# Performance work log

Measured on AMD Instinct MI355X. Metric: run time of the kernel, lower is better.

Reference implementation:

```python
import jax, jax.numpy as jnp
import numpy as np

N_STEPS = 8   # fixed-step RK4 surrogate for diffrax Dopri5 (same RHS math)
DT = 0.01     # dt0 used by the original module


def setup_inputs() -> dict:
    key = jax.random.key(0)
    ks = jax.random.split(key, 6)
    B, N, H = 16, 512, 128
    return {
        "y0": jax.random.normal(ks[0], (B, N), jnp.float32),
        "bias": jax.random.normal(ks[1], (B, N, 1), jnp.float32),
        "data_adj": jax.random.uniform(ks[2], (B, N, N), jnp.float32),
        "k0": jax.random.normal(ks[3], (H, N, N), jnp.float32) * 0.02,
        "k1": jax.random.normal(ks[4], (H, N, H), jnp.float32) * 0.02,
        "k2": jax.random.normal(ks[5], (N, N, H), jnp.float32) * 0.02,
    }


def reference(y0, bias, data_adj, k0, k1, k2):
    b = bias[..., 0]  # squeeze(bias, -1) -> [B, N]

    def rhs(y):
        z = y[..., None]  # [B, N, 1]
        # kernel chain: einsum('ijk,lmj->ilm') per layer (k summed out)
        z = jnp.einsum('ijk,lmj->ilm', z, k0)  # [B, H, N]
        z = jnp.einsum('ijk,lmj->ilm', z, k1)  # [B, H, N]
        z = jnp.einsum('ijk,lmj->ilm', z, k2)  # [B, N, N]
        z = jnp.sin(z)                          # Sine activation (dropout p=0 -> identity)
        agg = jnp.sum(data_adj * z, axis=-1)    # adjacency-masked reduction -> [B, N]
        return b - agg

    def step(y, _):
        r1 = rhs(y)
        r2 = rhs(y + 0.5 * DT * r1)
        r3 = rhs(y + 0.5 * DT * r2)
        r4 = rhs(y + DT * r3)
        y_new = y + (DT / 6.0) * (r1 + 2.0 * r2 + 2.0 * r3 + r4)
        return y_new, y_new

    _, ys = jax.lax.scan(step, y0, None, length=N_STEPS)
    return ys  # [N_STEPS, B, N] trajectory (SaveAt(ts=ts) analogue)
```

## Files before the change

kernel.cpp:

```cpp
#include <hip/hip_runtime.h>
#include <hip/hip_bf16.h>

typedef int int4v __attribute__((ext_vector_type(4)));
typedef long long i64;
typedef long long i64x2 __attribute__((ext_vector_type(2)));
typedef unsigned long long u64;
typedef unsigned int u32;

#define DT 0.01f

__device__ __forceinline__ float fast_sin(float x) {
  const float INVPI = 0.3183098861837907f;
  float n = rintf(x * INVPI);
  int ni = (int)n;
  float r = fmaf(n, -3.140625f, x);
  r = fmaf(n, -9.6765358979e-4f, r);
  float s = r * r;
  float p = fmaf(s, -2.5052108e-8f, 2.7557319e-6f);
  p = fmaf(s, p, -1.9841270e-4f);
  p = fmaf(s, p, 8.3333333e-3f);
  p = fmaf(s, p, -1.6666667e-1f);
  float res = fmaf(r * s, p, r);
  return (ni & 1) ? -res : res;
}

typedef float f32x16 __attribute__((ext_vector_type(16)));
__device__ __forceinline__ void sload4(const float* p, f32x16& a, f32x16& b,
                                       f32x16& c, f32x16& d) {
  asm volatile(
      "s_load_dwordx16 %0, %4, 0\n\t"
      "s_load_dwordx16 %1, %4, 0x40\n\t"
      "s_load_dwordx16 %2, %4, 0x80\n\t"
      "s_load_dwordx16 %3, %4, 0xc0\n\t"
      "s_waitcnt lgkmcnt(0)"
      : "=s"(a), "=s"(b), "=s"(c), "=s"(d)
      : "s"(p));
}

__global__ __launch_bounds__(256) void kPrep1(const float* __restrict__ k0,
                                              float* __restrict__ K0p) {
  const int id = (blockIdx.x & 255) * 256 + threadIdx.x;
  const int p = blockIdx.x >> 8;
  const int h = id >> 9, j = id & 511;
  const float* q = k0 + (size_t)h * 262144 + (size_t)(p * 256) * 512 + j;
  float s = 0.f;
  for (int m = 0; m < 256; ++m) s += q[(size_t)m * 512];
  K0p[p * 65536 + id] = s;
}

__global__ __launch_bounds__(256) void kPrep2(const float* __restrict__ k1,
                                              float* __restrict__ K1s) {
  int t = blockIdx.x * 256 + threadIdx.x;
  int h = t >> 7, j = t & 127;
  const float* p = k1 + (size_t)h * 65536 + j;
  float s = 0.f;
  for (int m = 0; m < 512; ++m) s += p[(size_t)m * 128];
  K1s[t] = s;
}

__global__ __launch_bounds__(256) void kPrep3(const float* __restrict__ K0p,
                                              const float* __restrict__ K1s,
                                              float* __restrict__ M) {
  int t = blockIdx.x * 256 + threadIdx.x;
  int l = t >> 9, j = t & 511;
  float s = 0.f;
#pragma unroll 8
  for (int h = 0; h < 128; ++h)
    s = fmaf(K1s[l * 128 + h], K0p[h * 512 + j] + K0p[65536 + h * 512 + j], s);
  M[t] = s;
}

__global__ __launch_bounds__(256) void kConvRow(const float* __restrict__ k2,
                                                i64x2* __restrict__ kF2,
                                                float* __restrict__ rowinv,
                                                float* __restrict__ crow) {
  const int t = threadIdx.x;
  const int row = blockIdx.x * 16 + (t >> 4);
  const int seg = t & 15;
  const float* src = k2 + (size_t)row * 128 + seg * 8;
  const float4 a = *(const float4*)(src);
  const float4 b = *(const float4*)(src + 4);
  float m = fmaxf(fmaxf(fmaxf(fabsf(a.x), fabsf(a.y)), fmaxf(fabsf(a.z), fabsf(a.w))),
                  fmaxf(fmaxf(fabsf(b.x), fabsf(b.y)), fmaxf(fabsf(b.z), fabsf(b.w))));
#pragma unroll
  for (int off = 8; off > 0; off >>= 1) m = fmaxf(m, __shfl_xor(m, off, 64));
  const float scale = m > 0.f ? 32767.0f / m : 0.f;
  if (seg == 0) rowinv[row] = m > 0.f ? m / 32767.0f : 0.f;
  const float v[8] = {a.x, a.y, a.z, a.w, b.x, b.y, b.z, b.w};
  u64 ph = 0, pl = 0;
  int csum = 0;
#pragma unroll
  for (int i = 0; i < 8; ++i) {
    const int q = (int)rintf(v[i] * scale);
    const int kh = q >> 8;
    const int kl = (q & 255) - 128;
    ph |= (u64)(unsigned char)(signed char)kh << (8 * i);
    pl |= (u64)(unsigned char)(signed char)kl << (8 * i);
    csum += q - 128;
  }
  i64x2 wv;
  wv.x = (i64)ph;
  wv.y = (i64)pl;
  kF2[((size_t)(row >> 4) * 4 + (seg >> 2)) * 64 + (seg & 3) * 16 + (row & 15)] = wv;
#pragma unroll
  for (int off = 8; off > 0; off >>= 1) csum += __shfl_xor(csum, off, 64);
  if (seg == 0) crow[row] = 32896.f * (float)csum;
}

__global__ __launch_bounds__(256) void kA2(
    const float* __restrict__ y0, const float* __restrict__ bias,
    const float* __restrict__ M, const float* __restrict__ aggp,
    float* __restrict__ ybuf, float* __restrict__ racc,
    float* __restrict__ s2T, float* __restrict__ out,
    int stage, int step) {
  __shared__ float ystage[512];
  const int b = blockIdx.x >> 4, lg = blockIdx.x & 15, t = threadIdx.x;
  const float* ycur = ybuf + (step & 1) * 8192;
  float* ynext = ybuf + ((step + 1) & 1) * 8192;

  for (int i = t; i < 512; i += 256) {
    const int idx = b * 512 + i;
    const bool own = (i >> 5) == lg;
    float ys;
    if (stage == 0) {
      ys = y0[idx];
      if (own) ynext[idx] = ys;
    } else {
      const float r = bias[idx] - (aggp[idx] + aggp[8192 + idx]);
      const float yb = ycur[idx];
      if (stage == 1) {
        ys = fmaf(0.5f * DT, r, yb);
        if (own) racc[idx] = r;
      } else if (stage == 2) {
        ys = fmaf(0.5f * DT, r, yb);
        if (own) racc[idx] = racc[idx] + 2.f * r;
      } else if (stage == 3) {
        ys = fmaf(DT, r, yb);
        if (own) racc[idx] = racc[idx] + 2.f * r;
      } else {
        ys = yb + (DT / 6.f) * (racc[idx] + r);
        if (own) { ynext[idx] = ys; out[step * 8192 + idx] = ys; }
      }
    }
    ystage[i] = ys;
  }
  __syncthreads();

  const int g = t >> 5, u = t & 31;
  const int l = lg * 8 + g;
  const float* Mrow = M + l * 512;
  const int i0 = u * 16;
  float p = 0.f;
#pragma unroll
  for (int k = 0; k < 4; ++k) {
    const int off = ((u + k) & 3) << 2;
    const float4 mv = *(const float4*)(Mrow + i0 + off);
    const float4 yv = *(const float4*)(ystage + i0 + off);
    p = fmaf(mv.x, yv.x, p);
    p = fmaf(mv.y, yv.y, p);
    p = fmaf(mv.z, yv.z, p);
    p = fmaf(mv.w, yv.w, p);
  }
#pragma unroll
  for (int off = 16; off > 0; off >>= 1) p += __shfl_down(p, off, 32);
  if (u == 0) s2T[l * 16 + b] = p;
}

__global__ __launch_bounds__(256) void kBi8(
    const i64x2* __restrict__ kF2,
    const float* __restrict__ adj, const float* __restrict__ s2T,
    const float* __restrict__ rowinv, const float* __restrict__ crow,
    float* __restrict__ aggp) {
  __shared__ __align__(8) signed char sqA[16][136];
  __shared__ __align__(8) signed char sqB[16][136];
  __shared__ __align__(8) signed char sqC[16][136];
  __shared__ float sred[16][16];
  __shared__ float scaleL[16], sinvLs[16], cbLs[16];
  __shared__ float part[64];
  const int t = threadIdx.x;
  const int b16 = t & 15, jg = t >> 4;

  float mx = 0.f;
#pragma unroll
  for (int i = 0; i < 8; ++i)
    mx = fmaxf(mx, fabsf(s2T[(jg * 8 + i) * 16 + b16]));
  sred[jg][b16] = mx;
  __syncthreads();
  if (t < 16) {
    float m = 0.f;
#pragma unroll
    for (int g = 0; g < 16; ++g) m = fmaxf(m, sred[g][t]);
    scaleL[t] = m > 0.f ? 8388607.f / m : 0.f;
    sinvLs[t] = m > 0.f ? m / 8388607.f : 0.f;
  }
  __syncthreads();
  {
    const float sc = scaleL[b16];
    u64 pa = 0, pb = 0, pc = 0;
    int ps2 = 0, psm = 0, psl = 0;
#pragma unroll
    for (int i = 0; i < 8; ++i) {
      int q = (int)rintf(s2T[(jg * 8 + i) * 16 + b16] * sc);
      q = q > 8388607 ? 8388607 : (q < -8388607 ? -8388607 : q);
      const int h = q >> 16;
      const int m = ((q >> 8) & 255) - 128;
      const int lo = (q & 255) - 128;
      pa |= (u64)(unsigned char)(signed char)h << (8 * i);
      pb |= (u64)(unsigned char)(signed char)m << (8 * i);
      pc |= (u64)(unsigned char)(signed char)lo << (8 * i);
      ps2 += h; psm += m; psl += lo;
    }
    *(u64*)&sqA[b16][jg * 8] = pa;
    *(u64*)&sqB[b16][jg * 8] = pb;
    *(u64*)&sqC[b16][jg * 8] = pc;
    sred[jg][b16] = 8388608.f * (float)ps2 + 32768.f * (float)psm + 128.f * (float)psl;
  }
  __syncthreads();
  if (t < 16) {
    float s = 0.f;
#pragma unroll
    for (int g = 0; g < 16; ++g) s += sred[g][t];
    cbLs[t] = s + 538968064.f;
  }
  __syncthreads();

  const int lane = t & 63, w = t >> 6;
  const int bb = lane & 15, kg = lane >> 4;
  i64 bA[4], bB[4], bC[4];
#pragma unroll
  for (int c = 0; c < 4; ++c) {
    const int kb = c * 32 + kg * 8;
    bA[c] = *(const i64*)&sqA[bb][kb];
    bB[c] = *(const i64*)&sqB[bb][kb];
    bC[c] = *(const i64*)&sqC[bb][kb];
  }
  const float sb = sinvLs[bb], cbb = cbLs[bb];

  const int rid0 = blockIdx.x * 256;
  const int l = rid0 >> 9;
  const int half = blockIdx.x & 1;

  float bacc = 0.f;
#pragma unroll
  for (int tt = 0; tt < 4; ++tt) {
    const int ridT = rid0 + w * 64 + tt * 16;
    const size_t tile = (size_t)(ridT >> 4);
    i64 ah[4], al[4];
#pragma unroll
    for (int c = 0; c < 4; ++c) {
      const i64x2 v = kF2[(tile * 4 + c) * 64 + lane];
      ah[c] = v.x;
      al[c] = v.y;
    }
    int4v Ga = {0, 0, 0, 0}, Gb = {0, 0, 0, 0}, Gc = {0, 0, 0, 0}, Gd = {0, 0, 0, 0};
#pragma unroll
    for (int c = 0; c < 4; ++c) {
      Ga = __builtin_amdgcn_mfma_i32_16x16x32_i8(ah[c], bA[c], Ga, 0, 0, 0);
      Gb = __builtin_amdgcn_mfma_i32_16x16x32_i8(ah[c], bB[c], Gb, 0, 0, 0);
      Gb = __builtin_amdgcn_mfma_i32_16x16x32_i8(al[c], bA[c], Gb, 0, 0, 0);
      Gc = __builtin_amdgcn_mfma_i32_16x16x32_i8(ah[c], bC[c], Gc, 0, 0, 0);
      Gc = __builtin_amdgcn_mfma_i32_16x16x32_i8(al[c], bB[c], Gc, 0, 0, 0);
      Gd = __builtin_amdgcn_mfma_i32_16x16x32_i8(al[c], bC[c], Gd, 0, 0, 0);
    }
    const int rbase = ridT + kg * 4;
    const float4 cr = *(const float4*)(crow + rbase);
    const float4 ri = *(const float4*)(rowinv + rbase);
    const float4 ad = *(const float4*)(adj + (size_t)bb * 262144 + rbase);
    const float crA[4] = {cr.x, cr.y, cr.z, cr.w};
    const float riA[4] = {ri.x, ri.y, ri.z, ri.w};
    const float adA[4] = {ad.x, ad.y, ad.z, ad.w};
    float ts = 0.f;
#pragma unroll
    for (int r = 0; r < 4; ++r) {
      const float dq = 16777216.f * (float)Ga[r] + 65536.f * (float)Gb[r] +
                       256.f * (float)Gc[r] + (float)Gd[r] + crA[r] + cbb;
      ts += adA[r] * fast_sin(dq * (riA[r] * sb));
    }
    ts += __shfl_xor(ts, 16, 64);
    ts += __shfl_xor(ts, 32, 64);
    bacc += ts;
  }
  if (lane < 16) part[w * 16 + lane] = bacc;
  __syncthreads();
  if (t < 16) {
    float ssum = part[t] + part[16 + t] + part[32 + t] + part[48 + t];
    aggp[half * 8192 + t * 512 + l] = ssum;
  }
}

__global__ __launch_bounds__(256) void kBf32(
    const float* __restrict__ k2, const float* __restrict__ adj,
    const float* __restrict__ s2T, float* __restrict__ aggp) {
  __shared__ float lk[256 * 36];
  __shared__ float part[64];
  const int t = threadIdx.x;
  const int rid0 = blockIdx.x * 256;
  const int rid = rid0 + t;
  const int l = rid0 >> 9;
  const int half = blockIdx.x & 1;

  float dot[16];
#pragma unroll
  for (int b = 0; b < 16; ++b) dot[b] = 0.f;

  for (int c = 0; c < 4; ++c) {
    __syncthreads();
#pragma unroll
    for (int k = 0; k < 8; ++k) {
      const int f = k * 256 + t, row = f >> 3, e = f & 7;
      const float4 v = *(const float4*)(k2 + (size_t)(rid0 + row) * 128 + c * 32 + e * 4);
      *(float4*)(lk + row * 36 + e * 4) = v;
    }
    __syncthreads();
    const float* myrow = lk + t * 36;
#pragma unroll
    for (int q = 0; q < 8; ++q) {
      const float4 kv = *(const float4*)(myrow + q * 4);
      f32x16 sa, sb, sc, sd;
      sload4(s2T + (c * 32 + q * 4) * 16, sa, sb, sc, sd);
#pragma unroll
      for (int b = 0; b < 16; ++b) dot[b] = fmaf(sa[b], kv.x, dot[b]);
#pragma unroll
      for (int b = 0; b < 16; ++b) dot[b] = fmaf(sb[b], kv.y, dot[b]);
#pragma unroll
      for (int b = 0; b < 16; ++b) dot[b] = fmaf(sc[b], kv.z, dot[b]);
#pragma unroll
      for (int b = 0; b < 16; ++b) dot[b] = fmaf(sd[b], kv.w, dot[b]);
    }
  }

#pragma unroll
  for (int b = 0; b < 16; ++b) {
    float v = adj[(size_t)b * 262144 + rid] * fast_sin(dot[b]);
#pragma unroll
    for (int off = 32; off > 0; off >>= 1) v += __shfl_down(v, off, 64);
    if ((t & 63) == 0) part[(t >> 6) * 16 + b] = v;
  }
  __syncthreads();
  if (t < 16) {
    float ssum = part[t] + part[16 + t] + part[32 + t] + part[48 + t];
    aggp[half * 8192 + t * 512 + l] = ssum;
  }
}

extern "C" void kernel_launch(void* const* d_in, const int* in_sizes, int n_in,
                              void* d_out, int out_size, void* d_ws, size_t ws_size,
                              hipStream_t stream) {
  const float* y0   = (const float*)d_in[0];
  const float* bias = (const float*)d_in[1];
  const float* adj  = (const float*)d_in[2];
  const float* k0   = (const float*)d_in[3];
  const float* k1   = (const float*)d_in[4];
  const float* k2   = (const float*)d_in[5];
  float* out = (float*)d_out;

  float* w      = (float*)d_ws;
  float* K0p    = w;
  float* K1s    = w + 131072;
  float* M      = w + 147456;
  float* s2T    = w + 212992;
  float* ybuf   = w + 215040;
  float* racc   = w + 231424;
  float* aggp   = w + 239616;
  float* rowinv = w + 256000;
  float* crow   = w + 518144;
  i64x2* kF2    = (i64x2*)(w + 780288);
  const bool useI8 =
      ws_size >= (size_t)780288 * 4 + (size_t)2 * 33554432;

  kPrep1<<<512, 256, 0, stream>>>(k0, K0p);
  kPrep2<<<64, 256, 0, stream>>>(k1, K1s);
  kPrep3<<<256, 256, 0, stream>>>(K0p, K1s, M);
  if (useI8) kConvRow<<<16384, 256, 0, stream>>>(k2, kF2, rowinv, crow);

  kA2<<<256, 256, 0, stream>>>(y0, bias, M, aggp, ybuf, racc, s2T, out, 0, -1);

  for (int step = 0; step < 8; ++step) {
    for (int stage = 1; stage <= 4; ++stage) {
      if (useI8)
        kBi8<<<1024, 256, 0, stream>>>(kF2, adj, s2T, rowinv, crow, aggp);
      else
        kBf32<<<1024, 256, 0, stream>>>(k2, adj, s2T, aggp);
      kA2<<<256, 256, 0, stream>>>(y0, bias, M, aggp, ybuf, racc, s2T, out, stage, step);
    }
  }
}
```

Measured before the change: 770.9 us.

## Quantize s2 in producer kernel using a precomputed norm bound, not per block

```diff
diff --git a/kernel.cpp b/kernel.cpp
--- a/kernel.cpp
+++ b/kernel.cpp
@@ -70,6 +70,26 @@
   M[t] = s;
 }
 
+__global__ __launch_bounds__(1024) void kNorm(const float* __restrict__ M,
+                                              float* __restrict__ Mnorm) {
+  __shared__ float red[128];
+  const int t = threadIdx.x;
+  const int l = t >> 3, seg = t & 7;
+  const float* row = M + l * 512 + seg * 64;
+  float s = 0.f;
+#pragma unroll 8
+  for (int i = 0; i < 64; ++i) s += fabsf(row[i]);
+#pragma unroll
+  for (int off = 4; off > 0; off >>= 1) s += __shfl_down(s, off, 8);
+  if (seg == 0) red[l] = s;
+  __syncthreads();
+  if (t == 0) {
+    float m = 0.f;
+    for (int i = 0; i < 128; ++i) m = fmaxf(m, red[i]);
+    Mnorm[0] = m;
+  }
+}
+
 __global__ __launch_bounds__(256) void kConvRow(const float* __restrict__ k2,
                                                 i64x2* __restrict__ kF2,
                                                 float* __restrict__ rowinv,
@@ -111,13 +131,21 @@
     const float* __restrict__ y0, const float* __restrict__ bias,
     const float* __restrict__ M, const float* __restrict__ aggp,
     float* __restrict__ ybuf, float* __restrict__ racc,
-    float* __restrict__ s2T, float* __restrict__ out,
+    float* __restrict__ s2T,
+    float* __restrict__ out,
+    const float* __restrict__ Mnorm,
+    signed char* __restrict__ sqG,
+    float* __restrict__ sinvB,
+    float* __restrict__ cbPart,
     int stage, int step) {
   __shared__ float ystage[512];
+  __shared__ float ymW[4];
+  __shared__ float red2[8];
   const int b = blockIdx.x >> 4, lg = blockIdx.x & 15, t = threadIdx.x;
   const float* ycur = ybuf + (step & 1) * 8192;
   float* ynext = ybuf + ((step + 1) & 1) * 8192;
 
+  float ay = 0.f;
   for (int i = t; i < 512; i += 256) {
     const int idx = b * 512 + i;
     const bool own = (i >> 5) == lg;
@@ -143,8 +171,17 @@
       }
     }
     ystage[i] = ys;
-  }
-  __syncthreads();
+    ay = fmaxf(ay, fabsf(ys));
+  }
+#pragma unroll
+  for (int off = 32; off > 0; off >>= 1) ay = fmaxf(ay, __shfl_xor(ay, off, 64));
+  if ((t & 63) == 0) ymW[t >> 6] = ay;
+  __syncthreads();
+
+  const float ymax = fmaxf(fmaxf(ymW[0], ymW[1]), fmaxf(ymW[2], ymW[3]));
+  const float bound = Mnorm[0] * ymax;
+  const float scaleB = bound > 0.f ? 8388607.f / bound : 0.f;
+  const float sinv = bound > 0.f ? bound / 8388607.f : 0.f;
 
   const int g = t >> 5, u = t & 31;
   const int l = lg * 8 + g;
@@ -163,78 +200,58 @@
   }
 #pragma unroll
   for (int off = 16; off > 0; off >>= 1) p += __shfl_down(p, off, 32);
-  if (u == 0) s2T[l * 16 + b] = p;
+  if (u == 0) {
+    s2T[l * 16 + b] = p;
+    int q = (int)rintf(p * scaleB);
+    q = q > 8388607 ? 8388607 : (q < -8388607 ? -8388607 : q);
+    const int sh = q >> 16;
+    const int sm = ((q >> 8) & 255) - 128;
+    const int sl = (q & 255) - 128;
+    sqG[b * 128 + l] = (signed char)sh;
+    sqG[2048 + b * 128 + l] = (signed char)sm;
+    sqG[4096 + b * 128 + l] = (signed char)sl;
+    red2[g] = 8388608.f * (float)sh + 32768.f * (float)sm + 128.f * (float)sl;
+  }
+  __syncthreads();
+  if (t == 0) {
+    float s = 0.f;
+#pragma unroll
+    for (int k = 0; k < 8; ++k) s += red2[k];
+    cbPart[b * 16 + lg] = s;
+    sinvB[b] = sinv;
+  }
 }
 
 __global__ __launch_bounds__(256) void kBi8(
     const i64x2* __restrict__ kF2,
-    const float* __restrict__ adj, const float* __restrict__ s2T,
+    const float* __restrict__ adj,
+    const signed char* __restrict__ sqG,
+    const float* __restrict__ sinvB, const float* __restrict__ cbPart,
     const float* __restrict__ rowinv, const float* __restrict__ crow,
     float* __restrict__ aggp) {
-  __shared__ __align__(8) signed char sqA[16][136];
-  __shared__ __align__(8) signed char sqB[16][136];
-  __shared__ __align__(8) signed char sqC[16][136];
-  __shared__ float sred[16][16];
-  __shared__ float scaleL[16], sinvLs[16], cbLs[16];
+  __shared__ float cbL[16];
   __shared__ float part[64];
   const int t = threadIdx.x;
-  const int b16 = t & 15, jg = t >> 4;
-
-  float mx = 0.f;
-#pragma unroll
-  for (int i = 0; i < 8; ++i)
-    mx = fmaxf(mx, fabsf(s2T[(jg * 8 + i) * 16 + b16]));
-  sred[jg][b16] = mx;
-  __syncthreads();
-  if (t < 16) {
-    float m = 0.f;
-#pragma unroll
-    for (int g = 0; g < 16; ++g) m = fmaxf(m, sred[g][t]);
-    scaleL[t] = m > 0.f ? 8388607.f / m : 0.f;
-    sinvLs[t] = m > 0.f ? m / 8388607.f : 0.f;
-  }
-  __syncthreads();
-  {
-    const float sc = scaleL[b16];
-    u64 pa = 0, pb = 0, pc = 0;
-    int ps2 = 0, psm = 0, psl = 0;
-#pragma unroll
-    for (int i = 0; i < 8; ++i) {
-      int q = (int)rintf(s2T[(jg * 8 + i) * 16 + b16] * sc);
-      q = q > 8388607 ? 8388607 : (q < -8388607 ? -8388607 : q);
-      const int h = q >> 16;
-      const int m = ((q >> 8) & 255) - 128;
-      const int lo = (q & 255) - 128;
-      pa |= (u64)(unsigned char)(signed char)h << (8 * i);
-      pb |= (u64)(unsigned char)(signed char)m << (8 * i);
-      pc |= (u64)(unsigned char)(signed char)lo << (8 * i);
-      ps2 += h; psm += m; psl += lo;
-    }
-    *(u64*)&sqA[b16][jg * 8] = pa;
-    *(u64*)&sqB[b16][jg * 8] = pb;
-    *(u64*)&sqC[b16][jg * 8] = pc;
-    sred[jg][b16] = 8388608.f * (float)ps2 + 32768.f * (float)psm + 128.f * (float)psl;
-  }
-  __syncthreads();
-  if (t < 16) {
-    float s = 0.f;
-#pragma unroll
-    for (int g = 0; g < 16; ++g) s += sred[g][t];
-    cbLs[t] = s + 538968064.f;
-  }
-  __syncthreads();
-
   const int lane = t & 63, w = t >> 6;
   const int bb = lane & 15, kg = lane >> 4;
+
+  if (t < 16) {
+    float s = 538968064.f;
+#pragma unroll
+    for (int g = 0; g < 16; ++g) s += cbPart[t * 16 + g];
+    cbL[t] = s;
+  }
+  __syncthreads();
+
   i64 bA[4], bB[4], bC[4];
 #pragma unroll
   for (int c = 0; c < 4; ++c) {
-    const int kb = c * 32 + kg * 8;
-    bA[c] = *(const i64*)&sqA[bb][kb];
-    bB[c] = *(const i64*)&sqB[bb][kb];
-    bC[c] = *(const i64*)&sqC[bb][kb];
-  }
-  const float sb = sinvLs[bb], cbb = cbLs[bb];
+    const int kb = bb * 128 + c * 32 + kg * 8;
+    bA[c] = *(const i64*)&sqG[kb];
+    bB[c] = *(const i64*)&sqG[2048 + kb];
+    bC[c] = *(const i64*)&sqG[4096 + kb];
+  }
+  const float sb = sinvB[bb], cbb = cbL[bb];
 
   const int rid0 = blockIdx.x * 256;
   const int l = rid0 >> 9;
@@ -358,30 +375,38 @@
   float* K0p    = w;
   float* K1s    = w + 131072;
   float* M      = w + 147456;
-  float* s2T    = w + 212992;
-  float* ybuf   = w + 215040;
-  float* racc   = w + 231424;
-  float* aggp   = w + 239616;
-  float* rowinv = w + 256000;
-  float* crow   = w + 518144;
-  i64x2* kF2    = (i64x2*)(w + 780288);
+  float* Mnorm  = w + 212992;
+  float* sinvB  = w + 213008;
+  float* cbPart = w + 213024;
+  float* s2T    = w + 213280;
+  float* ybuf   = w + 215328;
+  float* racc   = w + 231712;
+  float* aggp   = w + 239904;
+  signed char* sqG = (signed char*)(w + 256288);
+  float* rowinv = w + 257824;
+  float* crow   = w + 519968;
+  i64x2* kF2    = (i64x2*)(w + 782112);
   const bool useI8 =
-      ws_size >= (size_t)780288 * 4 + (size_t)2 * 33554432;
+      ws_size >= (size_t)782112 * 4 + (size_t)67108864;
 
   kPrep1<<<512, 256, 0, stream>>>(k0, K0p);
   kPrep2<<<64, 256, 0, stream>>>(k1, K1s);
   kPrep3<<<256, 256, 0, stream>>>(K0p, K1s, M);
+  kNorm<<<1, 1024, 0, stream>>>(M, Mnorm);
   if (useI8) kConvRow<<<16384, 256, 0, stream>>>(k2, kF2, rowinv, crow);
 
-  kA2<<<256, 256, 0, stream>>>(y0, bias, M, aggp, ybuf, racc, s2T, out, 0, -1);
+  kA2<<<256, 256, 0, stream>>>(y0, bias, M, aggp, ybuf, racc, s2T, out,
+                               Mnorm, sqG, sinvB, cbPart, 0, -1);
 
   for (int step = 0; step < 8; ++step) {
     for (int stage = 1; stage <= 4; ++stage) {
       if (useI8)
-        kBi8<<<1024, 256, 0, stream>>>(kF2, adj, s2T, rowinv, crow, aggp);
+        kBi8<<<1024, 256, 0, stream>>>(kF2, adj, sqG, sinvB, cbPart,
+                                       rowinv, crow, aggp);
       else
         kBf32<<<1024, 256, 0, stream>>>(k2, adj, s2T, aggp);
-      kA2<<<256, 256, 0, stream>>>(y0, bias, M, aggp, ybuf, racc, s2T, out, stage, step);
-    }
-  }
-}
+      kA2<<<256, 256, 0, stream>>>(y0, bias, M, aggp, ybuf, racc, s2T, out,
+                                   Mnorm, sqG, sinvB, cbPart, stage, step);
+    }
+  }
+}
```

After: 818.2 us. +6.1%, slower.
